# Kernel tuning notes

Hardware: AMD Instinct MI355X
Metric: run time of the kernel (lower is better)

## Reference

```python
import jax, jax.numpy as jnp
import numpy as np

NUM_CLASSES = 5  # sleep stages: W, N1, N2, N3, REM
N = 4194304


def setup_inputs() -> dict:
    key = jax.random.key(0)
    k1, k2 = jax.random.split(key)
    inputs = jax.random.normal(k1, (N, NUM_CLASSES), dtype=jnp.float32)
    targets = jax.random.randint(k2, (N,), 0, NUM_CLASSES, dtype=jnp.int32)
    return {"inputs": inputs, "targets": targets}


def reference(inputs, targets):
    # Mean False Error loss: per-class mean of per-sample cross-entropy,
    # summed over classes that are present in the batch.
    # per-sample CE loss (stable log-softmax, single pass)
    logp = jax.nn.log_softmax(inputs, axis=-1)                    # [N, C]
    per_sample = -jnp.take_along_axis(logp, targets[:, None].astype(jnp.int32), axis=1)[:, 0]  # [N]
    # segment-reduce by class label (replaces the python grouping loop)
    loss_sums = jax.ops.segment_sum(per_sample, targets, num_segments=NUM_CLASSES)             # [C]
    counts = jax.ops.segment_sum(jnp.ones_like(per_sample), targets, num_segments=NUM_CLASSES) # [C]
    # per-class mean; empty classes contribute 0
    means = jnp.where(counts > 0, loss_sums / jnp.maximum(counts, 1.0), 0.0)
    return jnp.sum(means)
```

## Files before the change

### kernel.cpp

```cpp
#include <hip/hip_runtime.h>

#define NCLS 5
#define NSAMP 4194304
#define BLOCK 256
#define GRID 2048
#define NTHREADS (GRID * BLOCK)
#define ITERS (NSAMP / (NTHREADS * 4))
#define NVALS (2 * NCLS)

__device__ __forceinline__ void accum_sample(float l0, float l1, float l2, float l3, float l4,
                                             int t, float sums[NCLS], unsigned int& packed_cnt) {
    float s = __expf(l0) + __expf(l1) + __expf(l2) + __expf(l3) + __expf(l4);
    float lt = (t == 0) ? l0 : (t == 1) ? l1 : (t == 2) ? l2 : (t == 3) ? l3 : l4;
    float ce = __logf(s) - lt;
#pragma unroll
    for (int k = 0; k < NCLS; ++k) {
        sums[k] += (t == k) ? ce : 0.0f;
    }
    packed_cnt += 1u << (6 * t);
}

__device__ __forceinline__ void block_reduce_10(float sums[NCLS], float cnts[NCLS],
                                                float* result10) {
#pragma unroll
    for (int k = 0; k < NCLS; ++k) {
#pragma unroll
        for (int off = 32; off > 0; off >>= 1) {
            sums[k] += __shfl_down(sums[k], off, 64);
            cnts[k] += __shfl_down(cnts[k], off, 64);
        }
    }
    __shared__ float ls[BLOCK / 64][NVALS];
    const int lane = threadIdx.x & 63;
    const int wave = threadIdx.x >> 6;
    if (lane == 0) {
#pragma unroll
        for (int k = 0; k < NCLS; ++k) {
            ls[wave][k] = sums[k];
            ls[wave][NCLS + k] = cnts[k];
        }
    }
    __syncthreads();
    if (threadIdx.x < NVALS) {
        float v = 0.f;
#pragma unroll
        for (int w = 0; w < BLOCK / 64; ++w) v += ls[w][threadIdx.x];
        *result10 = v;
    }
}

__global__ __launch_bounds__(BLOCK) void mfe_partial(const float* __restrict__ inputs,
                                                     const int* __restrict__ targets,
                                                     float* __restrict__ partial ) {
    const int tid = blockIdx.x * BLOCK + threadIdx.x;

    const int base0 = tid * 4;
    const int base1 = (NTHREADS + tid) * 4;
    const float4* p0 = (const float4*)(inputs + (size_t)base0 * NCLS);
    const float4* p1 = (const float4*)(inputs + (size_t)base1 * NCLS);
    float4 a0 = p0[0], b0 = p0[1], c0 = p0[2], d0 = p0[3], e0 = p0[4];
    float4 a1 = p1[0], b1 = p1[1], c1 = p1[2], d1 = p1[3], e1 = p1[4];
    int4 t0 = *(const int4*)(targets + base0);
    int4 t1 = *(const int4*)(targets + base1);

    float sums[NCLS] = {0.f, 0.f, 0.f, 0.f, 0.f};
    unsigned int packed = 0;

    accum_sample(a0.x, a0.y, a0.z, a0.w, b0.x, t0.x, sums, packed);
    accum_sample(b0.y, b0.z, b0.w, c0.x, c0.y, t0.y, sums, packed);
    accum_sample(c0.z, c0.w, d0.x, d0.y, d0.z, t0.z, sums, packed);
    accum_sample(d0.w, e0.x, e0.y, e0.z, e0.w, t0.w, sums, packed);
    accum_sample(a1.x, a1.y, a1.z, a1.w, b1.x, t1.x, sums, packed);
    accum_sample(b1.y, b1.z, b1.w, c1.x, c1.y, t1.y, sums, packed);
    accum_sample(c1.z, c1.w, d1.x, d1.y, d1.z, t1.z, sums, packed);
    accum_sample(d1.w, e1.x, e1.y, e1.z, e1.w, t1.w, sums, packed);

    float cnts[NCLS];
#pragma unroll
    for (int k = 0; k < NCLS; ++k) {
        cnts[k] = (float)((packed >> (6 * k)) & 63u);
    }

    float total;
    block_reduce_10(sums, cnts, &total);
    if (threadIdx.x < NVALS) {
        partial[threadIdx.x * GRID + blockIdx.x] = total;
    }
}

__global__ __launch_bounds__(BLOCK) void mfe_final(const float* __restrict__ partial,
                                                   float* __restrict__ out) {
    float sums[NCLS];
    float cnts[NCLS];
#pragma unroll
    for (int k = 0; k < NCLS; ++k) {
        float s = 0.f, c = 0.f;
#pragma unroll
        for (int i = 0; i < GRID / BLOCK; ++i) {
            s += partial[k * GRID + threadIdx.x + i * BLOCK];
            c += partial[(NCLS + k) * GRID + threadIdx.x + i * BLOCK];
        }
        sums[k] = s;
        cnts[k] = c;
    }

    float total;
    block_reduce_10(sums, cnts, &total);

    __shared__ float fin[NVALS];
    if (threadIdx.x < NVALS) fin[threadIdx.x] = total;
    __syncthreads();
    if (threadIdx.x == 0) {
        float loss = 0.f;
#pragma unroll
        for (int k = 0; k < NCLS; ++k) {
            float cnt = fin[NCLS + k];
            if (cnt > 0.f) loss += fin[k] / cnt;
        }
        out[0] = loss;
    }
}

extern "C" void kernel_launch(void* const* d_in, const int* in_sizes, int n_in,
                              void* d_out, int out_size, void* d_ws, size_t ws_size,
                              hipStream_t stream) {
    const float* inputs = (const float*)d_in[0];
    const int* targets = (const int*)d_in[1];
    float* out = (float*)d_out;
    float* partial = (float*)d_ws;

    mfe_partial<<<GRID, BLOCK, 0, stream>>>(inputs, targets, partial);
    mfe_final<<<1, BLOCK, 0, stream>>>(partial, out);
}
```

Baseline: 137.4 us.

## Fuse final reduction into partial kernel via last-block atomic counter

Merges the two-kernel reduction into a single kernel in which the last block to finish, found with an atomic counter and thread fences, performs the final cross-block sum and writes the loss. The final reads are also vectorised to float4. This removes the second kernel launch and its gap, but adds a memset launch to reset the counter plus a fence and atomic in every block.

Measured after the change: 233.5 us. +70.0%, slower.

```diff
diff --git a/kernel.cpp b/kernel.cpp
--- a/kernel.cpp
+++ b/kernel.cpp
@@ -5,7 +5,6 @@
 #define BLOCK 256
 #define GRID 2048
 #define NTHREADS (GRID * BLOCK)
-#define ITERS (NSAMP / (NTHREADS * 4))
 #define NVALS (2 * NCLS)
 
 __device__ __forceinline__ void accum_sample(float l0, float l1, float l2, float l3, float l4,
@@ -49,9 +48,11 @@
     }
 }
 
-__global__ __launch_bounds__(BLOCK) void mfe_partial(const float* __restrict__ inputs,
-                                                     const int* __restrict__ targets,
-                                                     float* __restrict__ partial ) {
+__global__ __launch_bounds__(BLOCK) void mfe_fused(const float* __restrict__ inputs,
+                                                   const int* __restrict__ targets,
+                                                   float* __restrict__ partial ,
+                                                   unsigned int* __restrict__ counter,
+                                                   float* __restrict__ out) {
     const int tid = blockIdx.x * BLOCK + threadIdx.x;
 
     const int base0 = tid * 4;
@@ -86,29 +87,35 @@
     if (threadIdx.x < NVALS) {
         partial[threadIdx.x * GRID + blockIdx.x] = total;
     }
-}
 
-__global__ __launch_bounds__(BLOCK) void mfe_final(const float* __restrict__ partial,
-                                                   float* __restrict__ out) {
-    float sums[NCLS];
-    float cnts[NCLS];
+    __shared__ int is_last;
+    if ((threadIdx.x >> 6) == 0) __threadfence();
+    __syncthreads();
+    if (threadIdx.x == 0) {
+        unsigned int old = atomicAdd(counter, 1u);
+        is_last = (old == GRID - 1u) ? 1 : 0;
+    }
+    __syncthreads();
+    if (!is_last) return;
+
+    __threadfence();
+    const float4* pp = (const float4*)partial;
+    float fsums[NCLS], fcnts[NCLS];
 #pragma unroll
     for (int k = 0; k < NCLS; ++k) {
-        float s = 0.f, c = 0.f;
-#pragma unroll
-        for (int i = 0; i < GRID / BLOCK; ++i) {
-            s += partial[k * GRID + threadIdx.x + i * BLOCK];
-            c += partial[(NCLS + k) * GRID + threadIdx.x + i * BLOCK];
-        }
-        sums[k] = s;
-        cnts[k] = c;
+        float4 v0 = pp[k * (GRID / 4) + threadIdx.x];
+        float4 v1 = pp[k * (GRID / 4) + BLOCK + threadIdx.x];
+        fsums[k] = (v0.x + v0.y) + (v0.z + v0.w) + (v1.x + v1.y) + (v1.z + v1.w);
+        float4 c0 = pp[(NCLS + k) * (GRID / 4) + threadIdx.x];
+        float4 c1 = pp[(NCLS + k) * (GRID / 4) + BLOCK + threadIdx.x];
+        fcnts[k] = (c0.x + c0.y) + (c0.z + c0.w) + (c1.x + c1.y) + (c1.z + c1.w);
     }
 
-    float total;
-    block_reduce_10(sums, cnts, &total);
+    float ftot;
+    block_reduce_10(fsums, fcnts, &ftot);
 
     __shared__ float fin[NVALS];
-    if (threadIdx.x < NVALS) fin[threadIdx.x] = total;
+    if (threadIdx.x < NVALS) fin[threadIdx.x] = ftot;
     __syncthreads();
     if (threadIdx.x == 0) {
         float loss = 0.f;
@@ -128,7 +135,9 @@
     const int* targets = (const int*)d_in[1];
     float* out = (float*)d_out;
     float* partial = (float*)d_ws;
+    unsigned int* counter =
+        (unsigned int*)((char*)d_ws + (size_t)NVALS * GRID * sizeof(float));
 
-    mfe_partial<<<GRID, BLOCK, 0, stream>>>(inputs, targets, partial);
-    mfe_final<<<1, BLOCK, 0, stream>>>(partial, out);
+    hipMemsetAsync(counter, 0, sizeof(unsigned int), stream);
+    mfe_fused<<<GRID, BLOCK, 0, stream>>>(inputs, targets, partial, counter, out);
 }
```
